# Kernel tuning notes

Measured on AMD Instinct MI355X. Metric: run time of the kernel, lower is better.

Reference implementation:

```python
import jax, jax.numpy as jnp
import numpy as np

EPS = 1e-5
NUM_HEADS = 8


def _ln(x, g, b):
    m = x.mean(-1, keepdims=True)
    v = jnp.mean((x - m) ** 2, -1, keepdims=True)
    return (x - m) * jax.lax.rsqrt(v + EPS) * g + b


def _bn(x, g, b, m, v):  # eval-mode BatchNorm2d on NCHW
    sh = (1, -1, 1, 1)
    return (x - m.reshape(sh)) * jax.lax.rsqrt(v.reshape(sh) + EPS) * g.reshape(sh) + b.reshape(sh)


def _conv3x3(x, w):
    return jax.lax.conv_general_dilated(x, w, (1, 1), 'SAME', dimension_numbers=('NCHW', 'OIHW', 'NCHW'))


def _gelu(x):
    return jax.nn.gelu(x, approximate=False)  # torch nn.GELU default (erf)


def _attention(x, w_qkv, temperature, w_proj):
    # XCiT-style cross-covariance (channel) attention
    B, N, C = x.shape
    h = NUM_HEADS
    d = C // h
    qkv = (x @ w_qkv.T).reshape(B, N, 3, h, d)
    qkv = jnp.transpose(qkv, (2, 0, 3, 4, 1))  # [3, B, h, d, N]
    q, k, v = qkv[0], qkv[1], qkv[2]
    q = q / jnp.maximum(jnp.linalg.norm(q, axis=-1, keepdims=True), 1e-12)
    k = k / jnp.maximum(jnp.linalg.norm(k, axis=-1, keepdims=True), 1e-12)
    attn = jnp.einsum('bhdn,bhen->bhde', q, k) * temperature[None, :, None, None]
    attn = jax.nn.softmax(attn, axis=-1)  # [B, h, d, d]
    out = jnp.einsum('bhde,bhen->bhdn', attn, v)
    out = jnp.transpose(out, (0, 3, 1, 2)).reshape(B, N, C)
    return out @ w_proj.T


def _forward(x, ln1_g, ln1_b, w_qkv, temperature, w_proj, gamma1,
             ln2_g, ln2_b, mlp_w1, bn1_g, bn1_b, bn1_m, bn1_v,
             mlp_w2, bn2_g, bn2_b, bn2_m, bn2_v, gamma2,
             ln3_g, ln3_b, pconv1, pbn_g, pbn_b, pbn_m, pbn_v, pconv2, gamma3,
             H, W):
    B, N, C = x.shape
    # --- Attention residual block ---
    z = _attention(_ln(x, ln1_g, ln1_b), w_qkv, temperature, w_proj)
    x = x + gamma1 * z
    # --- ConvMlp residual block (1x1 convs + eval BN) ---
    y = _ln(x, ln2_g, ln2_b)
    y = jnp.transpose(y, (0, 2, 1)).reshape(B, C, H, W)
    y = _bn(jnp.einsum('oc,bchw->bohw', mlp_w1, y), bn1_g, bn1_b, bn1_m, bn1_v)
    y = _gelu(y)
    y = _bn(jnp.einsum('oc,bchw->bohw', mlp_w2, y), bn2_g, bn2_b, bn2_m, bn2_v)
    y = jnp.transpose(y.reshape(B, C, N), (0, 2, 1))
    x = x + gamma2 * y
    # --- Projection residual block (3x3 conv + BN + GELU + 3x3 conv) ---
    p = _ln(x, ln3_g, ln3_b)
    p = jnp.transpose(p, (0, 2, 1)).reshape(B, C, H, W)
    p = _conv3x3(p, pconv1)
    p = _gelu(_bn(p, pbn_g, pbn_b, pbn_m, pbn_v))
    p = _conv3x3(p, pconv2)
    p = jnp.transpose(p.reshape(B, C, N), (0, 2, 1))
    x = x + gamma3 * p
    return x


def setup_inputs() -> dict:
    key = jax.random.key(0)
    B, H, W, C, MR = 16, 48, 48, 384, 2
    N = H * W
    C2 = C * MR
    ks = jax.random.split(key, 12)
    nrm = lambda k, sh, s: (jax.random.normal(k, sh) * s).astype(jnp.float32)
    INIT_VALUES = 1e-4  # ResidualBlock default gamma init
    return {
        'x': nrm(ks[0], (B, N, C), 1.0),
        'ln1_g': jnp.ones((C,), jnp.float32), 'ln1_b': jnp.zeros((C,), jnp.float32),
        'w_qkv': nrm(ks[1], (3 * C, C), C ** -0.5),
        'temperature': jnp.ones((NUM_HEADS,), jnp.float32),
        'w_proj': nrm(ks[2], (C, C), C ** -0.5),
        'gamma1': jnp.full((C,), INIT_VALUES, jnp.float32),
        'ln2_g': jnp.ones((C,), jnp.float32), 'ln2_b': jnp.zeros((C,), jnp.float32),
        'mlp_w1': nrm(ks[3], (C2, C), C ** -0.5),
        'bn1_g': jnp.ones((C2,), jnp.float32), 'bn1_b': jnp.zeros((C2,), jnp.float32),
        'bn1_m': nrm(ks[4], (C2,), 0.1), 'bn1_v': jnp.ones((C2,), jnp.float32),
        'mlp_w2': nrm(ks[5], (C, C2), C2 ** -0.5),
        'bn2_g': jnp.ones((C,), jnp.float32), 'bn2_b': jnp.zeros((C,), jnp.float32),
        'bn2_m': nrm(ks[6], (C,), 0.1), 'bn2_v': jnp.ones((C,), jnp.float32),
        'gamma2': jnp.full((C,), INIT_VALUES, jnp.float32),
        'ln3_g': jnp.ones((C,), jnp.float32), 'ln3_b': jnp.zeros((C,), jnp.float32),
        'pconv1': nrm(ks[7], (C, C, 3, 3), (9 * C) ** -0.5),
        'pbn_g': jnp.ones((C,), jnp.float32), 'pbn_b': jnp.zeros((C,), jnp.float32),
        'pbn_m': nrm(ks[8], (C,), 0.1), 'pbn_v': jnp.ones((C,), jnp.float32),
        'pconv2': nrm(ks[9], (C, C, 3, 3), (9 * C) ** -0.5),
        'gamma3': jnp.full((C,), INIT_VALUES, jnp.float32),
        'H': H, 'W': W,
    }


def reference(x, ln1_g, ln1_b, w_qkv, temperature, w_proj, gamma1,
              ln2_g, ln2_b, mlp_w1, bn1_g, bn1_b, bn1_m, bn1_v,
              mlp_w2, bn2_g, bn2_b, bn2_m, bn2_v, gamma2,
              ln3_g, ln3_b, pconv1, pbn_g, pbn_b, pbn_m, pbn_v, pconv2, gamma3,
              H, W):
    out = _forward(x, ln1_g, ln1_b, w_qkv, temperature, w_proj, gamma1,
                   ln2_g, ln2_b, mlp_w1, bn1_g, bn1_b, bn1_m, bn1_v,
                   mlp_w2, bn2_g, bn2_b, bn2_m, bn2_v, gamma2,
                   ln3_g, ln3_b, pconv1, pbn_g, pbn_b, pbn_m, pbn_v, pconv2, gamma3,
                   H, W)
    return (out, H, W)
```

## Files before the change

kernel.cpp:

```cpp
#include <hip/hip_runtime.h>
#include <hip/hip_bf16.h>

typedef unsigned short u16;
typedef unsigned char  u8;
typedef __attribute__((ext_vector_type(4))) float floatx4;

#define LN_EPS 1e-5f

__device__ __forceinline__ float bf2f(u16 u) {
    unsigned int i = ((unsigned int)u) << 16;
    float f; __builtin_memcpy(&f, &i, 4); return f;
}
__device__ __forceinline__ u16 f2bf(float f) {
    __hip_bfloat16 h = __float2bfloat16(f);
    u16 u; __builtin_memcpy(&u, &h, 2); return u;
}
__device__ __forceinline__ u8 f2e4(float f) {
    int p = __builtin_amdgcn_cvt_pk_fp8_f32(f, f, 0, false);
    return (u8)(p & 0xff);
}

__device__ __forceinline__ void gl_lds16(const u8* g, u8* l) {
    __builtin_amdgcn_global_load_lds(
        (const __attribute__((address_space(1))) void*)(const void*)g,
        (__attribute__((address_space(3))) void*)(void*)l,
        16, 0, 0);
}

__global__ void cvt_f2e4_kernel(const float* __restrict__ in, u8* __restrict__ out, int n4) {
    int i = blockIdx.x * blockDim.x + threadIdx.x;
    if (i < n4) {
        float4 f = ((const float4*)in)[i];
        uchar4 o; o.x = f2e4(f.x); o.y = f2e4(f.y); o.z = f2e4(f.z); o.w = f2e4(f.w);
        ((uchar4*)out)[i] = o;
    }
}

__global__ void zero_kernel(u16* __restrict__ p, int n) {
    int i = blockIdx.x * blockDim.x + threadIdx.x;
    if (i < n) p[i] = 0;
}

__global__ void zero_f32_kernel(float* __restrict__ p, int n) {
    int i = blockIdx.x * blockDim.x + threadIdx.x;
    if (i < n) p[i] = 0.f;
}

__global__ __launch_bounds__(64)
void ln_kernel(const float* __restrict__ xf, const float* __restrict__ g,
               const float* __restrict__ b, u8* __restrict__ out) {
    const int row = blockIdx.x;
    const int lane = threadIdx.x;
    const float* xr = xf + (size_t)row * 384;
    float v[6], s = 0.f, s2 = 0.f;
#pragma unroll
    for (int i = 0; i < 6; ++i) { v[i] = xr[lane + i * 64]; s += v[i]; s2 += v[i] * v[i]; }
#pragma unroll
    for (int off = 32; off; off >>= 1) { s += __shfl_xor(s, off); s2 += __shfl_xor(s2, off); }
    float mean = s * (1.0f / 384.0f);
    float var  = s2 * (1.0f / 384.0f) - mean * mean;
    float rstd = rsqrtf(var + LN_EPS);
    u8* orow = out + (size_t)row * 384;
#pragma unroll
    for (int i = 0; i < 6; ++i) {
        int c = lane + i * 64;
        orow[c] = f2e4((v[i] - mean) * rstd * g[c] + b[c]);
    }
}

template<int ACONV, int EPI>
__global__ __launch_bounds__(256, 4)
void gemm_nt(const u8* __restrict__ A, const u8* __restrict__ Bm,
             int M, int N, int K,
             u16* __restrict__ Obf, int ldo,
             float* __restrict__ xf, float* __restrict__ ofb, const float* __restrict__ xin,
             const float* __restrict__ bn_g, const float* __restrict__ bn_b,
             const float* __restrict__ bn_m, const float* __restrict__ bn_v,
             const float* __restrict__ gamma, const u8* __restrict__ zp) {
    __shared__ u8 As[2][128 * 64];
    __shared__ u8 Bs[2][128 * 64];

    const int tid = threadIdx.x;
    const int gx = gridDim.x;
    const int g  = blockIdx.y * gx + blockIdx.x;
    const int G  = gx * gridDim.y;
    int L = g;
    if ((G & 7) == 0) L = (g & 7) * (G >> 3) + (g >> 3);
    const int n0 = (L % gx) * 128;
    const int m0 = (L / gx) * 128;

    const int lane  = tid & 63;
    const int wave  = tid >> 6;
    const int wm    = (wave >> 1) * 64;
    const int wn    = (wave & 1) * 64;
    const int fr    = lane & 15;
    const int klane = lane >> 4;

    int arow[4], brow[4];
#pragma unroll
    for (int i = 0; i < 4; ++i) {
        arow[i] = (wm + i * 16 + fr) * 64;
        brow[i] = (wn + i * 16 + fr) * 64;
    }
    int csw[2];
#pragma unroll
    for (int kh = 0; kh < 2; ++kh)
        csw[kh] = ((((kh << 1) + (klane >> 1)) ^ (fr & 3)) << 4) + ((klane & 1) << 3);

    const int srow = tid >> 2;
    const int ssc  = (((tid & 3) ^ (srow & 3)) << 4);
    const u8 *sa[2], *sb[2];
    const u8* imgq[2];
    int ay[2], ax[2];
#pragma unroll
    for (int q = 0; q < 2; ++q) {
        int r = q * 64 + srow;
        if (ACONV == 0) {
            sa[q] = A + (size_t)(m0 + r) * K + ssc;
        } else {
            int nA = m0 + r;
            int bi = nA / 2304;
            int nl = nA - bi * 2304;
            ay[q] = nl / 48;
            ax[q] = nl - ay[q] * 48;
            imgq[q] = A + (size_t)bi * 2304 * 384;
        }
        sb[q] = Bm + (size_t)(n0 + q * 64 + srow) * K + ssc;
    }

    int scnt = 0, sjj = 0;
    const int NT = K / 64;

    auto STAGE = [&](int d) {
        if (ACONV == 1) {
            if (scnt == 0) {
                int t3 = sjj / 3;
                int dy = t3 - 1, dx = sjj - t3 * 3 - 1;
                ++sjj;
#pragma unroll
                for (int q = 0; q < 2; ++q) {
                    int yy = ay[q] + dy, xx = ax[q] + dx;
                    bool v = ((unsigned)yy < 48u) & ((unsigned)xx < 48u);
                    sa[q] = (v ? imgq[q] + (size_t)(yy * 48 + xx) * 384 : zp) + ssc;
                }
            }
            scnt = (scnt == 5) ? 0 : scnt + 1;
        }
        u8* la = &As[d][0];
        u8* lb = &Bs[d][0];
        gl_lds16(sa[0], la + ((wave * 64) << 4));        sa[0] += 64;
        gl_lds16(sa[1], la + ((256 + wave * 64) << 4));  sa[1] += 64;
        gl_lds16(sb[0], lb + ((wave * 64) << 4));        sb[0] += 64;
        gl_lds16(sb[1], lb + ((256 + wave * 64) << 4));  sb[1] += 64;
    };

    floatx4 acc[4][4];
#pragma unroll
    for (int i = 0; i < 4; ++i)
#pragma unroll
        for (int j = 0; j < 4; ++j) acc[i][j] = (floatx4){0.f, 0.f, 0.f, 0.f};

    STAGE(0);
    STAGE(1);
    asm volatile("s_waitcnt vmcnt(4)" ::: "memory");
    __builtin_amdgcn_s_barrier();
    asm volatile("" ::: "memory");

    int cur = 0;
    for (int t = 0; t < NT; ++t) {
        const u8* Ab = &As[cur][0];
        const u8* Bb = &Bs[cur][0];
#pragma unroll
        for (int kh = 0; kh < 2; ++kh) {
            long af[4], bfr[4];
#pragma unroll
            for (int i = 0; i < 4; ++i) af[i]  = *(const long*)(Ab + arow[i] + csw[kh]);
#pragma unroll
            for (int j = 0; j < 4; ++j) bfr[j] = *(const long*)(Bb + brow[j] + csw[kh]);
#pragma unroll
            for (int i = 0; i < 4; ++i)
#pragma unroll
                for (int j = 0; j < 4; ++j)
                    acc[i][j] = __builtin_amdgcn_mfma_f32_16x16x32_fp8_fp8(af[i], bfr[j], acc[i][j], 0, 0, 0);
        }
        asm volatile("s_waitcnt lgkmcnt(0)" ::: "memory");
        __builtin_amdgcn_s_barrier();
        asm volatile("" ::: "memory");
        if (t + 2 < NT) {
            STAGE(cur);
            asm volatile("s_waitcnt vmcnt(4)" ::: "memory");
        } else {
            asm volatile("s_waitcnt vmcnt(0)" ::: "memory");
        }
        __builtin_amdgcn_sched_barrier(0);
        __builtin_amdgcn_s_barrier();
        asm volatile("" ::: "memory");
        cur ^= 1;
    }

    const int quad4 = (lane >> 4) * 4;
#pragma unroll
    for (int j = 0; j < 4; ++j) {
        int col = n0 + wn + j * 16 + fr;
        float bscale = 0.f, bshift = 0.f, gam = 0.f;
        if (EPI == 1 || EPI == 2) {
            bscale = bn_g[col] * rsqrtf(bn_v[col] + LN_EPS);
            bshift = bn_b[col] - bn_m[col] * bscale;
        }
        if (EPI >= 2) gam = gamma[col];
#pragma unroll
        for (int i = 0; i < 4; ++i) {
#pragma unroll
            for (int r = 0; r < 4; ++r) {
                int row = m0 + wm + i * 16 + quad4 + r;
                float v = acc[i][j][r];
                if (EPI == 0) {
                    Obf[(size_t)row * ldo + col] = f2bf(v);
                } else if (EPI == 1) {
                    float t = v * bscale + bshift;
                    t = 0.5f * t * (1.0f + erff(t * 0.70710678118654752f));
                    ((u8*)Obf)[(size_t)row * ldo + col] = f2e4(t);
                } else if (EPI == 2) {
                    float t = v * bscale + bshift;
                    xf[(size_t)row * N + col] += gam * t;
                } else if (EPI == 3) {
                    xf[(size_t)row * N + col] += gam * v;
                } else if (EPI == 4) {
                    ofb[(size_t)row * N + col] = xf[(size_t)row * N + col] + gam * v;
                } else {
                    xf[(size_t)row * N + col] = xin[(size_t)row * N + col] + gam * v;
                }
            }
        }
    }
}

__global__ __launch_bounds__(256)
void gram_kernel(const u16* __restrict__ qkv, float* __restrict__ Sacc,
                 float* __restrict__ nrm2) {
    const int bh = blockIdx.y;
    const int b = bh >> 3, h = bh & 7;
    const int tid = threadIdx.x;
    __shared__ float qsf[64][48];
    __shared__ float ksf[64][48];

    float acc9[3][3];
#pragma unroll
    for (int i = 0; i < 3; ++i)
#pragma unroll
        for (int j = 0; j < 3; ++j) acc9[i][j] = 0.f;
    float qn2 = 0.f, kn2 = 0.f;

    const int qoff = h * 48;
    const int koff = 384 + h * 48;
    const int d0 = (tid >> 4) * 3;
    const int e0 = (tid & 15) * 3;
    const int nbase = blockIdx.x * 128;

    for (int c = 0; c < 2; ++c) {
        const int n0 = nbase + c * 64;
#pragma unroll
        for (int it = 0; it < 6; ++it) {
            int chunk = tid + it * 256;
            int mat = chunk >= 768 ? 1 : 0;
            int rem = chunk - mat * 768;
            int nn = rem / 12, u = rem - nn * 12;
            ushort4 raw = *(const ushort4*)(qkv + (size_t)(b * 2304 + n0 + nn) * 1152 +
                                            (mat ? koff : qoff) + u * 4);
            float4 f = make_float4(bf2f(raw.x), bf2f(raw.y), bf2f(raw.z), bf2f(raw.w));
            if (mat) *(float4*)&ksf[nn][u * 4] = f;
            else     *(float4*)&qsf[nn][u * 4] = f;
        }
        __syncthreads();
#pragma unroll 4
        for (int nn = 0; nn < 64; ++nn) {
            float q0 = qsf[nn][d0], q1 = qsf[nn][d0 + 1], q2 = qsf[nn][d0 + 2];
            float k0v = ksf[nn][e0], k1v = ksf[nn][e0 + 1], k2v = ksf[nn][e0 + 2];
            acc9[0][0] += q0 * k0v; acc9[0][1] += q0 * k1v; acc9[0][2] += q0 * k2v;
            acc9[1][0] += q1 * k0v; acc9[1][1] += q1 * k1v; acc9[1][2] += q1 * k2v;
            acc9[2][0] += q2 * k0v; acc9[2][1] += q2 * k1v; acc9[2][2] += q2 * k2v;
        }
        if (tid < 48) {
            for (int nn = 0; nn < 64; ++nn) { float q = qsf[nn][tid]; qn2 += q * q; }
        } else if (tid >= 128 && tid < 176) {
            int e = tid - 128;
            for (int nn = 0; nn < 64; ++nn) { float k = ksf[nn][e]; kn2 += k * k; }
        }
        __syncthreads();
    }

    float* Sb = Sacc + (size_t)bh * 2304;
#pragma unroll
    for (int i = 0; i < 3; ++i)
#pragma unroll
        for (int j = 0; j < 3; ++j)
            atomicAdd(&Sb[(d0 + i) * 48 + e0 + j], acc9[i][j]);
    if (tid < 48) atomicAdd(&nrm2[bh * 96 + tid], qn2);
    else if (tid >= 128 && tid < 176) atomicAdd(&nrm2[bh * 96 + 48 + (tid - 128)], kn2);
}

__global__ __launch_bounds__(256)
void attn_fin_kernel(const float* __restrict__ Sacc, const float* __restrict__ nrm2,
                     const float* __restrict__ temp, float* __restrict__ attnb) {
    const int bh = blockIdx.x;
    const int h = bh & 7;
    const int tid = threadIdx.x;
    __shared__ float S[48][49];
    __shared__ float qns[48], kns[48];

    const float* Sb = Sacc + (size_t)bh * 2304;
    for (int i = tid; i < 2304; i += 256) {
        int d = i / 48, e = i - d * 48;
        S[d][e] = Sb[i];
    }
    if (tid < 48)      qns[tid]      = fmaxf(sqrtf(nrm2[bh * 96 + tid]), 1e-12f);
    else if (tid < 96) kns[tid - 48] = fmaxf(sqrtf(nrm2[bh * 96 + tid]), 1e-12f);
    __syncthreads();

    if (tid < 48) {
        float tf = temp[h] / qns[tid];
        float mx = -1e30f;
        for (int e = 0; e < 48; ++e) {
            float t = S[tid][e] * tf / kns[e];
            S[tid][e] = t;
            mx = fmaxf(mx, t);
        }
        float sum = 0.f;
        for (int e = 0; e < 48; ++e) { float t = __expf(S[tid][e] - mx); S[tid][e] = t; sum += t; }
        float inv = 1.0f / sum;
        float* dst = attnb + ((size_t)bh * 48 + tid) * 48;
        for (int e = 0; e < 48; ++e) dst[e] = S[tid][e] * inv;
    }
}

__global__ __launch_bounds__(256)
void attnout_kernel(const u16* __restrict__ qkv, const float* __restrict__ attnb,
                    u8* __restrict__ z) {
    const int r0 = blockIdx.x * 64;
    const int h  = blockIdx.y;
    const int b  = r0 / 2304;
    const int tid = threadIdx.x;
    __shared__ float A[48][49];
    __shared__ float vsf[64][48];

    const float* asrc = attnb + (size_t)(b * 8 + h) * 2304;
    for (int i = tid; i < 2304; i += 256) {
        int d = i / 48, e = i - d * 48;
        A[d][e] = asrc[i];
    }
    const int voff = 768 + h * 48;
    for (int i = tid; i < 768; i += 256) {
        int nn = i / 12, u = i - nn * 12;
        ushort4 raw = *(const ushort4*)(qkv + (size_t)(r0 + nn) * 1152 + voff + u * 4);
        float4 f = make_float4(bf2f(raw.x), bf2f(raw.y), bf2f(raw.z), bf2f(raw.w));
        *(float4*)&vsf[nn][u * 4] = f;
    }
    __syncthreads();

    const int rr0 = (tid >> 4) * 4;
    const int d0  = (tid & 15) * 3;
    float acc[4][3];
#pragma unroll
    for (int r = 0; r < 4; ++r)
#pragma unroll
        for (int j = 0; j < 3; ++j) acc[r][j] = 0.f;

#pragma unroll 4
    for (int e = 0; e < 48; ++e) {
        float a0 = A[d0][e], a1 = A[d0 + 1][e], a2 = A[d0 + 2][e];
#pragma unroll
        for (int r = 0; r < 4; ++r) {
            float vv = vsf[rr0 + r][e];
            acc[r][0] += a0 * vv; acc[r][1] += a1 * vv; acc[r][2] += a2 * vv;
        }
    }
#pragma unroll
    for (int r = 0; r < 4; ++r)
#pragma unroll
        for (int j = 0; j < 3; ++j)
            z[(size_t)(r0 + rr0 + r) * 384 + h * 48 + d0 + j] = f2e4(acc[r][j]);
}

__global__ void reorder_w_kernel(const float* __restrict__ w, u8* __restrict__ wr, int n) {
    int i = blockIdx.x * blockDim.x + threadIdx.x;
    if (i < n) {
        int o = i / 3456, rem = i - o * 3456;
        int j = rem / 384, c = rem - j * 384;
        wr[i] = f2e4(w[(size_t)(o * 384 + c) * 9 + j]);
    }
}

__global__ void tail_kernel(const int* __restrict__ Hp, const int* __restrict__ Wp,
                            float* __restrict__ out, size_t base, int n_extra) {
    if (threadIdx.x == 0) {
        if (n_extra >= 1) out[base]     = (float)Hp[0];
        if (n_extra >= 2) out[base + 1] = (float)Wp[0];
    }
}

extern "C" void kernel_launch(void* const* d_in, const int* in_sizes, int n_in,
                              void* d_out, int out_size, void* d_ws, size_t ws_size,
                              hipStream_t stream) {
    const float* x      = (const float*)d_in[0];
    const float* ln1_g  = (const float*)d_in[1];
    const float* ln1_b  = (const float*)d_in[2];
    const float* w_qkv  = (const float*)d_in[3];
    const float* temp   = (const float*)d_in[4];
    const float* w_proj = (const float*)d_in[5];
    const float* gamma1 = (const float*)d_in[6];
    const float* ln2_g  = (const float*)d_in[7];
    const float* ln2_b  = (const float*)d_in[8];
    const float* mlp_w1 = (const float*)d_in[9];
    const float* bn1_g  = (const float*)d_in[10];
    const float* bn1_b  = (const float*)d_in[11];
    const float* bn1_m  = (const float*)d_in[12];
    const float* bn1_v  = (const float*)d_in[13];
    const float* mlp_w2 = (const float*)d_in[14];
    const float* bn2_g  = (const float*)d_in[15];
    const float* bn2_b  = (const float*)d_in[16];
    const float* bn2_m  = (const float*)d_in[17];
    const float* bn2_v  = (const float*)d_in[18];
    const float* gamma2 = (const float*)d_in[19];
    const float* ln3_g  = (const float*)d_in[20];
    const float* ln3_b  = (const float*)d_in[21];
    const float* pconv1 = (const float*)d_in[22];
    const float* pbn_g  = (const float*)d_in[23];
    const float* pbn_b  = (const float*)d_in[24];
    const float* pbn_m  = (const float*)d_in[25];
    const float* pbn_v  = (const float*)d_in[26];
    const float* pconv2 = (const float*)d_in[27];
    const float* gamma3 = (const float*)d_in[28];
    const int* Hp = (const int*)d_in[29];
    const int* Wp = (const int*)d_in[30];

    const int M = 36864, C = 384, C2 = 768, NQKV = 1152, KC = 3456;
    const size_t NBNC = (size_t)M * C;

    const size_t SZ_XF  = NBNC * 4;
    const size_t SZ_LN  = NBNC * 2;
    const size_t SZ_BIG = (size_t)M * NQKV * 2;
    const size_t SZ_P3  = SZ_LN;
    const size_t SZ_W   = (size_t)C * KC * 2;
    if (ws_size < SZ_XF + SZ_LN + SZ_BIG + SZ_P3 + 2 * SZ_W) return;

    char* ws = (char*)d_ws;
    float* xf     = (float*)ws;
    u8*    lnbuf  = (u8*)(ws + SZ_XF);
    u16*   big    = (u16*)(ws + SZ_XF + SZ_LN);
    char*  p3     = ws + SZ_XF + SZ_LN + SZ_BIG;
    float* attnb  = (float*)p3;
    u8*    wqkvb  = (u8*)(p3 + 1179648);
    u8*    wprojb = (u8*)(p3 + 1179648 + 884736);
    u8*    w1b    = (u8*)(p3 + 1179648 + 884736 + 294912);
    u8*    w2b    = (u8*)(p3 + 1179648 + 884736 + 294912 + 589824);
    float* Sacc   = (float*)(p3 + 3538944);
    float* nrm2   = (float*)(p3 + 3538944 + 1179648);
    u8*    convbf = (u8*)p3;
    u8*    w1r    = (u8*)(p3 + SZ_P3);
    u8*    w2r    = (u8*)(p3 + SZ_P3 + SZ_W);
    u8*    zp     = (u8*)big;

    const int n_extra = out_size - (int)NBNC;

    cvt_f2e4_kernel<<<(NQKV * C / 4 + 255) / 256, 256, 0, stream>>>(w_qkv, wqkvb, NQKV * C / 4);
    cvt_f2e4_kernel<<<(C * C / 4 + 255) / 256, 256, 0, stream>>>(w_proj, wprojb, C * C / 4);
    cvt_f2e4_kernel<<<(C2 * C / 4 + 255) / 256, 256, 0, stream>>>(mlp_w1, w1b, C2 * C / 4);
    cvt_f2e4_kernel<<<(C * C2 / 4 + 255) / 256, 256, 0, stream>>>(mlp_w2, w2b, C * C2 / 4);
    zero_f32_kernel<<<(128 * 2304 + 128 * 96 + 255) / 256, 256, 0, stream>>>(
        Sacc, 128 * 2304 + 128 * 96);

    ln_kernel<<<M, 64, 0, stream>>>(x, ln1_g, ln1_b, lnbuf);
    gemm_nt<0, 0><<<dim3(NQKV / 128, M / 128), 256, 0, stream>>>(
        lnbuf, wqkvb, M, NQKV, C, big, NQKV, nullptr, nullptr, nullptr,
        nullptr, nullptr, nullptr, nullptr, nullptr, nullptr);
    gram_kernel<<<dim3(18, 128), 256, 0, stream>>>(big, Sacc, nrm2);
    attn_fin_kernel<<<128, 256, 0, stream>>>(Sacc, nrm2, temp, attnb);
    attnout_kernel<<<dim3(M / 64, 8), 256, 0, stream>>>(big, attnb, lnbuf);
    gemm_nt<0, 5><<<dim3(C / 128, M / 128), 256, 0, stream>>>(
        lnbuf, wprojb, M, C, C, nullptr, 0, xf, nullptr, x,
        nullptr, nullptr, nullptr, nullptr, gamma1, nullptr);

    ln_kernel<<<M, 64, 0, stream>>>(xf, ln2_g, ln2_b, lnbuf);
    gemm_nt<0, 1><<<dim3(C2 / 128, M / 128), 256, 0, stream>>>(
        lnbuf, w1b, M, C2, C, (u16*)big, C2, nullptr, nullptr, nullptr,
        bn1_g, bn1_b, bn1_m, bn1_v, nullptr, nullptr);
    gemm_nt<0, 2><<<dim3(C / 128, M / 128), 256, 0, stream>>>(
        (u8*)big, w2b, M, C, C2, nullptr, 0, xf, nullptr, nullptr,
        bn2_g, bn2_b, bn2_m, bn2_v, gamma2, nullptr);

    ln_kernel<<<M, 64, 0, stream>>>(xf, ln3_g, ln3_b, lnbuf);
    reorder_w_kernel<<<(C * KC + 255) / 256, 256, 0, stream>>>(pconv1, w1r, C * KC);
    reorder_w_kernel<<<(C * KC + 255) / 256, 256, 0, stream>>>(pconv2, w2r, C * KC);
    zero_kernel<<<8, 256, 0, stream>>>((u16*)zp, 2048);
    gemm_nt<1, 1><<<dim3(C / 128, M / 128), 256, 0, stream>>>(
        lnbuf, w1r, M, C, KC, (u16*)convbf, C, nullptr, nullptr, nullptr,
        pbn_g, pbn_b, pbn_m, pbn_v, nullptr, zp);
    gemm_nt<1, 4><<<dim3(C / 128, M / 128), 256, 0, stream>>>(
        convbf, w2r, M, C, KC, nullptr, 0, xf, (float*)d_out, nullptr,
        nullptr, nullptr, nullptr, nullptr, gamma3, zp);

    tail_kernel<<<1, 64, 0, stream>>>(Hp, Wp, (float*)d_out, NBNC, n_extra);
}
```

Measured before the change: 743.0 us.

## Add 256-row M-tile GEMM variant for linear layers and rotate LDS swizzle

Adds a BIGM template path where each block computes a 256x128 tile (each wave 128x64 with 8x4 MFMA fragments) and uses it for the QKV, projection and MLP GEMMs. Occupancy drops to 2 blocks per CU. The conv GEMMs keep the 128x128 tile. The LDS swizzle for both staging and fragment reads changes from XOR to a rotation pattern. The larger tile is meant to improve B-operand reuse and cut global traffic per FLOP, at the cost of more registers, more LDS, fewer blocks and possible tail imbalance.

```diff
diff --git a/kernel.cpp b/kernel.cpp
--- a/kernel.cpp
+++ b/kernel.cpp
@@ -68,8 +68,8 @@
     }
 }
 
-template<int ACONV, int EPI>
-__global__ __launch_bounds__(256, 4)
+template<int ACONV, int EPI, bool BIGM>
+__global__ __launch_bounds__(256, BIGM ? 2 : 4)
 void gemm_nt(const u8* __restrict__ A, const u8* __restrict__ Bm,
              int M, int N, int K,
              u16* __restrict__ Obf, int ldo,
@@ -77,7 +77,10 @@
              const float* __restrict__ bn_g, const float* __restrict__ bn_b,
              const float* __restrict__ bn_m, const float* __restrict__ bn_v,
              const float* __restrict__ gamma, const u8* __restrict__ zp) {
-    __shared__ u8 As[2][128 * 64];
+    constexpr int BM = BIGM ? 256 : 128;
+    constexpr int AQ = BIGM ? 4 : 2;
+    constexpr int MI = BIGM ? 8 : 4;
+    __shared__ u8 As[2][BM * 64];
     __shared__ u8 Bs[2][128 * 64];
 
     const int tid = threadIdx.x;
@@ -87,33 +90,32 @@
     int L = g;
     if ((G & 7) == 0) L = (g & 7) * (G >> 3) + (g >> 3);
     const int n0 = (L % gx) * 128;
-    const int m0 = (L / gx) * 128;
+    const int m0 = (L / gx) * BM;
 
     const int lane  = tid & 63;
     const int wave  = tid >> 6;
-    const int wm    = (wave >> 1) * 64;
+    const int wm    = BIGM ? ((wave >> 1) * 128) : ((wave >> 1) * 64);
     const int wn    = (wave & 1) * 64;
     const int fr    = lane & 15;
     const int klane = lane >> 4;
 
-    int arow[4], brow[4];
-#pragma unroll
-    for (int i = 0; i < 4; ++i) {
-        arow[i] = (wm + i * 16 + fr) * 64;
-        brow[i] = (wn + i * 16 + fr) * 64;
-    }
+    int arow[MI], brow[4];
+#pragma unroll
+    for (int i = 0; i < MI; ++i) arow[i] = (wm + i * 16 + fr) * 64;
+#pragma unroll
+    for (int j = 0; j < 4; ++j)  brow[j] = (wn + j * 16 + fr) * 64;
     int csw[2];
 #pragma unroll
     for (int kh = 0; kh < 2; ++kh)
-        csw[kh] = ((((kh << 1) + (klane >> 1)) ^ (fr & 3)) << 4) + ((klane & 1) << 3);
+        csw[kh] = ((((kh << 1) + (klane >> 1) + (fr >> 1)) & 3) << 4) + ((klane & 1) << 3);
 
     const int srow = tid >> 2;
-    const int ssc  = (((tid & 3) ^ (srow & 3)) << 4);
-    const u8 *sa[2], *sb[2];
-    const u8* imgq[2];
-    int ay[2], ax[2];
-#pragma unroll
-    for (int q = 0; q < 2; ++q) {
+    const int ssc  = ((((tid & 3) - ((tid >> 3) & 3)) & 3) << 4);
+    const u8 *sa[AQ], *sb[2];
+    const u8* imgq[AQ];
+    int ay[AQ], ax[AQ];
+#pragma unroll
+    for (int q = 0; q < AQ; ++q) {
         int r = q * 64 + srow;
         if (ACONV == 0) {
             sa[q] = A + (size_t)(m0 + r) * K + ssc;
@@ -125,8 +127,10 @@
             ax[q] = nl - ay[q] * 48;
             imgq[q] = A + (size_t)bi * 2304 * 384;
         }
+    }
+#pragma unroll
+    for (int q = 0; q < 2; ++q)
         sb[q] = Bm + (size_t)(n0 + q * 64 + srow) * K + ssc;
-    }
 
     int scnt = 0, sjj = 0;
     const int NT = K / 64;
@@ -138,7 +142,7 @@
                 int dy = t3 - 1, dx = sjj - t3 * 3 - 1;
                 ++sjj;
 #pragma unroll
-                for (int q = 0; q < 2; ++q) {
+                for (int q = 0; q < AQ; ++q) {
                     int yy = ay[q] + dy, xx = ax[q] + dx;
                     bool v = ((unsigned)yy < 48u) & ((unsigned)xx < 48u);
                     sa[q] = (v ? imgq[q] + (size_t)(yy * 48 + xx) * 384 : zp) + ssc;
@@ -148,21 +152,22 @@
         }
         u8* la = &As[d][0];
         u8* lb = &Bs[d][0];
-        gl_lds16(sa[0], la + ((wave * 64) << 4));        sa[0] += 64;
-        gl_lds16(sa[1], la + ((256 + wave * 64) << 4));  sa[1] += 64;
-        gl_lds16(sb[0], lb + ((wave * 64) << 4));        sb[0] += 64;
-        gl_lds16(sb[1], lb + ((256 + wave * 64) << 4));  sb[1] += 64;
+#pragma unroll
+        for (int q = 0; q < AQ; ++q) { gl_lds16(sa[q], la + ((q * 256 + wave * 64) << 4)); sa[q] += 64; }
+#pragma unroll
+        for (int q = 0; q < 2; ++q)  { gl_lds16(sb[q], lb + ((q * 256 + wave * 64) << 4)); sb[q] += 64; }
     };
 
-    floatx4 acc[4][4];
-#pragma unroll
-    for (int i = 0; i < 4; ++i)
+    floatx4 acc[MI][4];
+#pragma unroll
+    for (int i = 0; i < MI; ++i)
 #pragma unroll
         for (int j = 0; j < 4; ++j) acc[i][j] = (floatx4){0.f, 0.f, 0.f, 0.f};
 
     STAGE(0);
     STAGE(1);
-    asm volatile("s_waitcnt vmcnt(4)" ::: "memory");
+    if constexpr (BIGM) asm volatile("s_waitcnt vmcnt(6)" ::: "memory");
+    else                asm volatile("s_waitcnt vmcnt(4)" ::: "memory");
     __builtin_amdgcn_s_barrier();
     asm volatile("" ::: "memory");
 
@@ -172,13 +177,13 @@
         const u8* Bb = &Bs[cur][0];
 #pragma unroll
         for (int kh = 0; kh < 2; ++kh) {
-            long af[4], bfr[4];
-#pragma unroll
-            for (int i = 0; i < 4; ++i) af[i]  = *(const long*)(Ab + arow[i] + csw[kh]);
-#pragma unroll
-            for (int j = 0; j < 4; ++j) bfr[j] = *(const long*)(Bb + brow[j] + csw[kh]);
-#pragma unroll
-            for (int i = 0; i < 4; ++i)
+            long af[MI], bfr[4];
+#pragma unroll
+            for (int i = 0; i < MI; ++i) af[i]  = *(const long*)(Ab + arow[i] + csw[kh]);
+#pragma unroll
+            for (int j = 0; j < 4; ++j)  bfr[j] = *(const long*)(Bb + brow[j] + csw[kh]);
+#pragma unroll
+            for (int i = 0; i < MI; ++i)
 #pragma unroll
                 for (int j = 0; j < 4; ++j)
                     acc[i][j] = __builtin_amdgcn_mfma_f32_16x16x32_fp8_fp8(af[i], bfr[j], acc[i][j], 0, 0, 0);
@@ -188,7 +193,8 @@
         asm volatile("" ::: "memory");
         if (t + 2 < NT) {
             STAGE(cur);
-            asm volatile("s_waitcnt vmcnt(4)" ::: "memory");
+            if constexpr (BIGM) asm volatile("s_waitcnt vmcnt(6)" ::: "memory");
+            else                asm volatile("s_waitcnt vmcnt(4)" ::: "memory");
         } else {
             asm volatile("s_waitcnt vmcnt(0)" ::: "memory");
         }
@@ -209,7 +215,7 @@
         }
         if (EPI >= 2) gam = gamma[col];
 #pragma unroll
-        for (int i = 0; i < 4; ++i) {
+        for (int i = 0; i < MI; ++i) {
 #pragma unroll
             for (int r = 0; r < 4; ++r) {
                 int row = m0 + wm + i * 16 + quad4 + r;
@@ -470,21 +476,21 @@
         Sacc, 128 * 2304 + 128 * 96);
 
     ln_kernel<<<M, 64, 0, stream>>>(x, ln1_g, ln1_b, lnbuf);
-    gemm_nt<0, 0><<<dim3(NQKV / 128, M / 128), 256, 0, stream>>>(
+    gemm_nt<0, 0, true><<<dim3(NQKV / 128, M / 256), 256, 0, stream>>>(
         lnbuf, wqkvb, M, NQKV, C, big, NQKV, nullptr, nullptr, nullptr,
         nullptr, nullptr, nullptr, nullptr, nullptr, nullptr);
     gram_kernel<<<dim3(18, 128), 256, 0, stream>>>(big, Sacc, nrm2);
     attn_fin_kernel<<<128, 256, 0, stream>>>(Sacc, nrm2, temp, attnb);
     attnout_kernel<<<dim3(M / 64, 8), 256, 0, stream>>>(big, attnb, lnbuf);
-    gemm_nt<0, 5><<<dim3(C / 128, M / 128), 256, 0, stream>>>(
+    gemm_nt<0, 5, true><<<dim3(C / 128, M / 256), 256, 0, stream>>>(
         lnbuf, wprojb, M, C, C, nullptr, 0, xf, nullptr, x,
         nullptr, nullptr, nullptr, nullptr, gamma1, nullptr);
 
     ln_kernel<<<M, 64, 0, stream>>>(xf, ln2_g, ln2_b, lnbuf);
-    gemm_nt<0, 1><<<dim3(C2 / 128, M / 128), 256, 0, stream>>>(
+    gemm_nt<0, 1, true><<<dim3(C2 / 128, M / 256), 256, 0, stream>>>(
         lnbuf, w1b, M, C2, C, (u16*)big, C2, nullptr, nullptr, nullptr,
         bn1_g, bn1_b, bn1_m, bn1_v, nullptr, nullptr);
-    gemm_nt<0, 2><<<dim3(C / 128, M / 128), 256, 0, stream>>>(
+    gemm_nt<0, 2, true><<<dim3(C / 128, M / 256), 256, 0, stream>>>(
         (u8*)big, w2b, M, C, C2, nullptr, 0, xf, nullptr, nullptr,
         bn2_g, bn2_b, bn2_m, bn2_v, gamma2, nullptr);
 
@@ -492,10 +498,10 @@
     reorder_w_kernel<<<(C * KC + 255) / 256, 256, 0, stream>>>(pconv1, w1r, C * KC);
     reorder_w_kernel<<<(C * KC + 255) / 256, 256, 0, stream>>>(pconv2, w2r, C * KC);
     zero_kernel<<<8, 256, 0, stream>>>((u16*)zp, 2048);
-    gemm_nt<1, 1><<<dim3(C / 128, M / 128), 256, 0, stream>>>(
+    gemm_nt<1, 1, false><<<dim3(C / 128, M / 128), 256, 0, stream>>>(
         lnbuf, w1r, M, C, KC, (u16*)convbf, C, nullptr, nullptr, nullptr,
         pbn_g, pbn_b, pbn_m, pbn_v, nullptr, zp);
-    gemm_nt<1, 4><<<dim3(C / 128, M / 128), 256, 0, stream>>>(
+    gemm_nt<1, 4, false><<<dim3(C / 128, M / 128), 256, 0, stream>>>(
         convbf, w2r, M, C, KC, nullptr, 0, xf, (float*)d_out, nullptr,
         nullptr, nullptr, nullptr, nullptr, gamma3, zp);
 
```

New measurement: 732.7 us. No clear change (-1.4%).

## Pre-swizzle fp8 operands in global memory to avoid LDS bank conflicts

Applied to the files above, without the earlier changes.

Moves the LDS bank-conflict swizzle from the load path into the producers. The weight converters, LayerNorm, the GELU epilogue and the attention output kernel now write fp8 rows with an 8-byte chunk permutation keyed on the row index. The GEMM loads linearly into LDS and reads fragments with a matching permuted column offset, recomputed per 3x3 tap for the conv path. This aims to cut bank conflicts on the 8-byte fragment reads, but it couples every producer to the GEMM's layout and adds index arithmetic in the conv inner loop.

```diff
diff --git a/kernel.cpp b/kernel.cpp
--- a/kernel.cpp
+++ b/kernel.cpp
@@ -18,6 +18,10 @@
 __device__ __forceinline__ u8 f2e4(float f) {
     int p = __builtin_amdgcn_cvt_pk_fp8_f32(f, f, 0, false);
     return (u8)(p & 0xff);
+}
+
+__device__ __forceinline__ int swz(int m, int k) {
+    return (k & ~63) | (((((k >> 3) + (m >> 1)) & 7) << 3)) | (k & 7);
 }
 
 __device__ __forceinline__ void gl_lds16(const u8* g, u8* l) {
@@ -27,12 +31,15 @@
         16, 0, 0);
 }
 
-__global__ void cvt_f2e4_kernel(const float* __restrict__ in, u8* __restrict__ out, int n4) {
+__global__ void cvt_f2e4_kernel(const float* __restrict__ in, u8* __restrict__ out,
+                                int n4, int Kp) {
     int i = blockIdx.x * blockDim.x + threadIdx.x;
     if (i < n4) {
         float4 f = ((const float4*)in)[i];
         uchar4 o; o.x = f2e4(f.x); o.y = f2e4(f.y); o.z = f2e4(f.z); o.w = f2e4(f.w);
-        ((uchar4*)out)[i] = o;
+        int e = i * 4;
+        int n = e / Kp, k = e - n * Kp;
+        *(uchar4*)(out + (size_t)n * Kp + swz(n, k)) = o;
     }
 }
 
@@ -61,10 +68,12 @@
     float var  = s2 * (1.0f / 384.0f) - mean * mean;
     float rstd = rsqrtf(var + LN_EPS);
     u8* orow = out + (size_t)row * 384;
+    const int gperm = (row >> 1) & 7;
+    const int pofs = ((((lane >> 3) + gperm) & 7) << 3) | (lane & 7);
 #pragma unroll
     for (int i = 0; i < 6; ++i) {
         int c = lane + i * 64;
-        orow[c] = f2e4((v[i] - mean) * rstd * g[c] + b[c]);
+        orow[i * 64 + pofs] = f2e4((v[i] - mean) * rstd * g[c] + b[c]);
     }
 }
 
@@ -96,6 +105,9 @@
     const int fr    = lane & 15;
     const int klane = lane >> 4;
 
+    const int hE = fr >> 1;
+    const int hO = ((fr + 1) >> 1) & 7;
+
     int arow[4], brow[4];
 #pragma unroll
     for (int i = 0; i < 4; ++i) {
@@ -105,10 +117,11 @@
     int csw[2];
 #pragma unroll
     for (int kh = 0; kh < 2; ++kh)
-        csw[kh] = ((((kh << 1) + (klane >> 1)) ^ (fr & 3)) << 4) + ((klane & 1) << 3);
+        csw[kh] = ((((kh << 2) + klane) + hE) & 7) << 3;
+    int cswA[2] = { csw[0], csw[1] };
 
     const int srow = tid >> 2;
-    const int ssc  = (((tid & 3) ^ (srow & 3)) << 4);
+    const int scol = (tid & 3) << 4;
     const u8 *sa[2], *sb[2];
     const u8* imgq[2];
     int ay[2], ax[2];
@@ -116,7 +129,7 @@
     for (int q = 0; q < 2; ++q) {
         int r = q * 64 + srow;
         if (ACONV == 0) {
-            sa[q] = A + (size_t)(m0 + r) * K + ssc;
+            sa[q] = A + (size_t)(m0 + r) * K + scol;
         } else {
             int nA = m0 + r;
             int bi = nA / 2304;
@@ -125,7 +138,7 @@
             ax[q] = nl - ay[q] * 48;
             imgq[q] = A + (size_t)bi * 2304 * 384;
         }
-        sb[q] = Bm + (size_t)(n0 + q * 64 + srow) * K + ssc;
+        sb[q] = Bm + (size_t)(n0 + q * 64 + srow) * K + scol;
     }
 
     int scnt = 0, sjj = 0;
@@ -141,7 +154,7 @@
                 for (int q = 0; q < 2; ++q) {
                     int yy = ay[q] + dy, xx = ax[q] + dx;
                     bool v = ((unsigned)yy < 48u) & ((unsigned)xx < 48u);
-                    sa[q] = (v ? imgq[q] + (size_t)(yy * 48 + xx) * 384 : zp) + ssc;
+                    sa[q] = (v ? imgq[q] + (size_t)(yy * 48 + xx) * 384 : zp) + scol;
                 }
             }
             scnt = (scnt == 5) ? 0 : scnt + 1;
@@ -166,17 +179,31 @@
     __builtin_amdgcn_s_barrier();
     asm volatile("" ::: "memory");
 
+    int rcnt = 0, rtap = 0;
     int cur = 0;
     for (int t = 0; t < NT; ++t) {
+        if (ACONV == 1) {
+            if (rcnt == 0) {
+                int t3 = rtap / 3;
+                int dy = t3 - 1, dx = rtap - t3 * 3 - 1;
+                ++rtap;
+                int Cp = m0 + dy * 48 + dx + 4608;
+                int cc = (Cp >> 1) & 7;
+                int h  = (Cp & 1) ? hO : hE;
+                cswA[0] = ((klane + h + cc) & 7) << 3;
+                cswA[1] = ((4 + klane + h + cc) & 7) << 3;
+            }
+            rcnt = (rcnt == 5) ? 0 : rcnt + 1;
+        }
         const u8* Ab = &As[cur][0];
         const u8* Bb = &Bs[cur][0];
 #pragma unroll
         for (int kh = 0; kh < 2; ++kh) {
             long af[4], bfr[4];
 #pragma unroll
-            for (int i = 0; i < 4; ++i) af[i]  = *(const long*)(Ab + arow[i] + csw[kh]);
-#pragma unroll
-            for (int j = 0; j < 4; ++j) bfr[j] = *(const long*)(Bb + brow[j] + csw[kh]);
+            for (int i = 0; i < 4; ++i) af[i]  = *(const long*)(Ab + arow[i] + (ACONV ? cswA[kh] : csw[kh]));
+#pragma unroll
+            for (int j = 0; j < 4; ++j)  bfr[j] = *(const long*)(Bb + brow[j] + csw[kh]);
 #pragma unroll
             for (int i = 0; i < 4; ++i)
 #pragma unroll
@@ -219,7 +246,7 @@
                 } else if (EPI == 1) {
                     float t = v * bscale + bshift;
                     t = 0.5f * t * (1.0f + erff(t * 0.70710678118654752f));
-                    ((u8*)Obf)[(size_t)row * ldo + col] = f2e4(t);
+                    ((u8*)Obf)[(size_t)row * ldo + swz(row, col)] = f2e4(t);
                 } else if (EPI == 2) {
                     float t = v * bscale + bshift;
                     xf[(size_t)row * N + col] += gam * t;
@@ -377,8 +404,11 @@
 #pragma unroll
     for (int r = 0; r < 4; ++r)
 #pragma unroll
-        for (int j = 0; j < 3; ++j)
-            z[(size_t)(r0 + rr0 + r) * 384 + h * 48 + d0 + j] = f2e4(acc[r][j]);
+        for (int j = 0; j < 3; ++j) {
+            int row = r0 + rr0 + r;
+            int col = h * 48 + d0 + j;
+            z[(size_t)row * 384 + swz(row, col)] = f2e4(acc[r][j]);
+        }
 }
 
 __global__ void reorder_w_kernel(const float* __restrict__ w, u8* __restrict__ wr, int n) {
@@ -386,7 +416,7 @@
     if (i < n) {
         int o = i / 3456, rem = i - o * 3456;
         int j = rem / 384, c = rem - j * 384;
-        wr[i] = f2e4(w[(size_t)(o * 384 + c) * 9 + j]);
+        wr[(size_t)o * 3456 + swz(o, rem)] = f2e4(w[(size_t)(o * 384 + c) * 9 + j]);
     }
 }
 
@@ -462,10 +492,10 @@
 
     const int n_extra = out_size - (int)NBNC;
 
-    cvt_f2e4_kernel<<<(NQKV * C / 4 + 255) / 256, 256, 0, stream>>>(w_qkv, wqkvb, NQKV * C / 4);
-    cvt_f2e4_kernel<<<(C * C / 4 + 255) / 256, 256, 0, stream>>>(w_proj, wprojb, C * C / 4);
-    cvt_f2e4_kernel<<<(C2 * C / 4 + 255) / 256, 256, 0, stream>>>(mlp_w1, w1b, C2 * C / 4);
-    cvt_f2e4_kernel<<<(C * C2 / 4 + 255) / 256, 256, 0, stream>>>(mlp_w2, w2b, C * C2 / 4);
+    cvt_f2e4_kernel<<<(NQKV * C / 4 + 255) / 256, 256, 0, stream>>>(w_qkv, wqkvb, NQKV * C / 4, C);
+    cvt_f2e4_kernel<<<(C * C / 4 + 255) / 256, 256, 0, stream>>>(w_proj, wprojb, C * C / 4, C);
+    cvt_f2e4_kernel<<<(C2 * C / 4 + 255) / 256, 256, 0, stream>>>(mlp_w1, w1b, C2 * C / 4, C);
+    cvt_f2e4_kernel<<<(C * C2 / 4 + 255) / 256, 256, 0, stream>>>(mlp_w2, w2b, C * C2 / 4, C2);
     zero_f32_kernel<<<(128 * 2304 + 128 * 96 + 255) / 256, 256, 0, stream>>>(
         Sacc, 128 * 2304 + 128 * 96);
 
```

After: 744.0 us. No clear change (+0.1%).
